# Optimization experiments

Measured on AMD Instinct MI355X. Metric: run time of the kernel, lower is better.

Reference implementation:

```python
import jax, jax.numpy as jnp
import numpy as np

H = 16
D_MODEL = 1024
D_K = D_MODEL // H  # 64, must equal embeddim


def setup_inputs() -> dict:
    key = jax.random.key(0)
    ks = jax.random.split(key, 20)
    B, S, D = 4, 1024, D_MODEL
    s = 0.02
    inp = {
        'query': jax.random.normal(ks[0], (B, S, D), jnp.float32),
        'key':   jax.random.normal(ks[1], (B, S, D), jnp.float32),
        'value': jax.random.normal(ks[2], (B, S, D), jnp.float32),
        'mask':  jnp.ones((B, S, S), jnp.int32),
        # four d_model x d_model projections (q, k, v, out)
        'wq': jax.random.normal(ks[3], (D, D), jnp.float32) * s, 'bq': jnp.zeros((D,), jnp.float32),
        'wk': jax.random.normal(ks[4], (D, D), jnp.float32) * s, 'bk': jnp.zeros((D,), jnp.float32),
        'wv': jax.random.normal(ks[5], (D, D), jnp.float32) * s, 'bv': jnp.zeros((D,), jnp.float32),
        'wo': jax.random.normal(ks[6], (D, D), jnp.float32) * s, 'bo': jnp.zeros((D,), jnp.float32),
        # per-head (embeddim=64) linears
        'spatial_w': jax.random.normal(ks[7], (D_K, D_K), jnp.float32) * s, 'spatial_b': jnp.zeros((D_K,), jnp.float32),
        'qproj_w':   jax.random.normal(ks[8], (D_K, D_K), jnp.float32) * s, 'qproj_b':   jnp.zeros((D_K,), jnp.float32),
        'kproj_w':   jax.random.normal(ks[9], (D_K, D_K), jnp.float32) * s, 'kproj_b':   jnp.zeros((D_K,), jnp.float32),
        'vlin_w':    jax.random.normal(ks[10], (D_K, D_K), jnp.float32) * s, 'vlin_b':    jnp.zeros((D_K,), jnp.float32),
        # channel_linear: Linear(1, 64)
        'chan_w': jax.random.normal(ks[11], (1, D_K), jnp.float32) * s, 'chan_b': jnp.zeros((D_K,), jnp.float32),
    }
    return inp


def reference(query, key, value, mask,
              wq, bq, wk, bk, wv, bv, wo, bo,
              spatial_w, spatial_b, qproj_w, qproj_b,
              kproj_w, kproj_b, vlin_w, vlin_b, chan_w, chan_b):
    B, S, D = query.shape
    # project and split heads -> [B, H, S, D_K]
    def heads(x, w, b):
        return (x @ w + b).reshape(B, S, H, D_K).transpose(0, 2, 1, 3)
    q = heads(query, wq, bq)
    k = heads(key, wk, bk)
    v = heads(value, wv, bv)

    q = jax.nn.elu(q @ spatial_w + spatial_b)
    q_refine = q @ qproj_w + qproj_b
    # channel gate: mean over channels -> Linear(1,64) -> matmul with raw key
    alpha = q_refine.mean(-1, keepdims=True) @ chan_w + chan_b        # [B,H,S,64]
    gate = jax.nn.sigmoid(jnp.einsum('bhqe,bhke->bhqk', alpha, k))    # [B,H,S,S]

    k2 = jax.nn.elu(k @ kproj_w + kproj_b)
    scores = jnp.einsum('bhqe,bhke->bhqk', q, k2) / jnp.sqrt(jnp.asarray(D_K, q.dtype))
    scores = scores * gate
    scores = jnp.where(mask[:, None] == 0, jnp.asarray(-1e9, scores.dtype), scores)
    p_attn = jax.nn.softmax(scores, axis=-1)

    v2 = jax.nn.elu(v @ vlin_w + vlin_b)
    x = jnp.einsum('bhqk,bhke->bhqe', p_attn, v2)                     # [B,H,S,64]
    x = x.transpose(0, 2, 1, 3).reshape(B, S, H * D_K)
    return x @ wo + bo
```

## Files before the change

### kernel.cpp

```cpp
#include <hip/hip_runtime.h>
#include <math.h>

#define D_MODEL 1024
#define NH 16
#define DK 64
#define S_LEN 1024
#define BATCH 4
#define MROWS (BATCH * S_LEN)

typedef short bf16x8 __attribute__((ext_vector_type(8)));
typedef float f32x4 __attribute__((ext_vector_type(4)));
typedef unsigned short u16;

__device__ __forceinline__ float elu1(float x) {
    return x > 0.f ? x : (expf(x) - 1.f);
}

__device__ __forceinline__ u16 f2bf(float f) {
    union { float f; unsigned u; } v; v.f = f;
    unsigned u = v.u;
    return (u16)((u + 0x7fffu + ((u >> 16) & 1u)) >> 16);
}

__device__ __forceinline__ float bf2f(u16 h) {
    union { unsigned u; float f; } v; v.u = ((unsigned)h) << 16;
    return v.f;
}

__device__ __forceinline__ unsigned pack2(float a, float b) {
    union { float f; unsigned u; } ua, ub; ua.f = a; ub.f = b;
    return ((ua.u + 0x8000u) >> 16) | ((ub.u + 0x8000u) & 0xffff0000u);
}

__device__ __forceinline__ void async16(const void* g, void* l) {
    __builtin_amdgcn_global_load_lds(
        (const __attribute__((address_space(1))) unsigned int*)g,
        (__attribute__((address_space(3))) unsigned int*)l,
        16, 0, 0);
}

__global__ __launch_bounds__(256) void cast_wt(
    const float* __restrict__ wq, const float* __restrict__ wk,
    const float* __restrict__ wv, const float* __restrict__ wo,
    u16* __restrict__ WT)
{
    __shared__ float T[64][65];
    const int z = blockIdx.z;
    const float* W = (z == 0) ? wq : ((z == 1) ? wk : ((z == 2) ? wv : wo));
    u16* O = WT + (size_t)z * D_MODEL * D_MODEL;
    const int tid = threadIdx.x;
    const int k0 = blockIdx.y * 64, n0 = blockIdx.x * 64;
    const int r = tid >> 4, c4 = (tid & 15) * 4;
    #pragma unroll
    for (int p = 0; p < 4; p++) {
        float4 v = *(const float4*)&W[(size_t)(k0 + r + p * 16) * D_MODEL + n0 + c4];
        T[r + p * 16][c4 + 0] = v.x; T[r + p * 16][c4 + 1] = v.y;
        T[r + p * 16][c4 + 2] = v.z; T[r + p * 16][c4 + 3] = v.w;
    }
    __syncthreads();
    #pragma unroll
    for (int p = 0; p < 4; p++) {
        const int i = r + p * 16;
        ushort4 o4;
        o4.x = f2bf(T[c4 + 0][i]); o4.y = f2bf(T[c4 + 1][i]);
        o4.z = f2bf(T[c4 + 2][i]); o4.w = f2bf(T[c4 + 3][i]);
        *(ushort4*)&O[(size_t)(n0 + i) * D_MODEL + k0 + c4] = o4;
    }
}

__global__ __launch_bounds__(256) void proj_gemm(
    const float* __restrict__ Xq, const float* __restrict__ Xk, const float* __restrict__ Xv,
    const u16* __restrict__ WTq, const u16* __restrict__ WTk, const u16* __restrict__ WTv,
    const float* __restrict__ bq, const float* __restrict__ bk, const float* __restrict__ bv,
    u16* __restrict__ Pbuf)
{
    __shared__ u16 As[128 * 32];
    __shared__ u16 Bs[128 * 32];

    const int z = blockIdx.z;
    const float* X = (z == 0) ? Xq : ((z == 1) ? Xk : Xv);
    const u16* WT = (z == 0) ? WTq : ((z == 1) ? WTk : WTv);
    const float* bias = (z == 0) ? bq : ((z == 1) ? bk : bv);
    u16* C = Pbuf + (size_t)z * MROWS * D_MODEL;

    const int tid = threadIdx.x;
    const int wave = tid >> 6, lane = tid & 63;
    const int col = lane & 15, quad = lane >> 4;
    const int wr = wave >> 1, wc = wave & 1;
    const int n0 = blockIdx.x * 128, r0 = blockIdx.y * 128;

    const int arow = tid >> 1, ahalf = tid & 1;
    const float* aptr = X + (size_t)(r0 + arow) * D_MODEL + ahalf * 16;
    u16* adst = As + arow * 32 + ahalf * 16;

    const int ch0 = 2 * wave, ch1 = 2 * wave + 1;
    const u16* bptr0 = WT + (size_t)(n0 + ch0 * 16 + (lane >> 2)) * D_MODEL + (lane & 3) * 8;
    const u16* bptr1 = WT + (size_t)(n0 + ch1 * 16 + (lane >> 2)) * D_MODEL + (lane & 3) * 8;
    u16* bdst0 = Bs + ch0 * 512;
    u16* bdst1 = Bs + ch1 * 512;

    f32x4 acc[4][4];
    #pragma unroll
    for (int i = 0; i < 4; i++)
        #pragma unroll
        for (int j = 0; j < 4; j++)
            acc[i][j] = (f32x4){0.f, 0.f, 0.f, 0.f};

    float4 f0 = *(const float4*)(aptr);
    float4 f1 = *(const float4*)(aptr + 4);
    float4 f2 = *(const float4*)(aptr + 8);
    float4 f3 = *(const float4*)(aptr + 12);

    for (int k0 = 0; k0 < D_MODEL; k0 += 32) {
        if (k0) __syncthreads();
        async16(bptr0 + k0, bdst0);
        async16(bptr1 + k0, bdst1);
        {
            uint4 p0, p1;
            p0.x = pack2(f0.x, f0.y); p0.y = pack2(f0.z, f0.w);
            p0.z = pack2(f1.x, f1.y); p0.w = pack2(f1.z, f1.w);
            p1.x = pack2(f2.x, f2.y); p1.y = pack2(f2.z, f2.w);
            p1.z = pack2(f3.x, f3.y); p1.w = pack2(f3.z, f3.w);
            *(uint4*)adst = p0;
            *(uint4*)(adst + 8) = p1;
        }
        if (k0 + 32 < D_MODEL) {
            const float* ap = aptr + k0 + 32;
            f0 = *(const float4*)(ap);
            f1 = *(const float4*)(ap + 4);
            f2 = *(const float4*)(ap + 8);
            f3 = *(const float4*)(ap + 12);
        }
        __syncthreads();
        const u16* Ab = As + (wr * 64 + col) * 32 + quad * 8;
        const u16* Bb = Bs + (wc * 64 + col) * 32 + quad * 8;
        bf16x8 af[4], bfr[4];
        #pragma unroll
        for (int mi = 0; mi < 4; mi++) af[mi] = *(const bf16x8*)(Ab + mi * 512);
        #pragma unroll
        for (int ni = 0; ni < 4; ni++) bfr[ni] = *(const bf16x8*)(Bb + ni * 512);
        #pragma unroll
        for (int mi = 0; mi < 4; mi++)
            #pragma unroll
            for (int ni = 0; ni < 4; ni++)
                acc[mi][ni] = __builtin_amdgcn_mfma_f32_16x16x32_bf16(af[mi], bfr[ni], acc[mi][ni], 0, 0, 0);
    }

    #pragma unroll
    for (int mi = 0; mi < 4; mi++)
        #pragma unroll
        for (int ni = 0; ni < 4; ni++) {
            const int gr = r0 + wr * 64 + mi * 16 + quad * 4;
            const int gc = n0 + wc * 64 + ni * 16 + col;
            const float bb = bias[gc];
            #pragma unroll
            for (int r = 0; r < 4; r++)
                C[(size_t)(gr + r) * D_MODEL + gc] = f2bf(acc[mi][ni][r] + bb);
        }
}

__global__ __launch_bounds__(256) void head_post(
    const u16* Pbuf, u16* QK2buf,
    const float* __restrict__ spatial_w, const float* __restrict__ spatial_b,
    const float* __restrict__ qproj_w, const float* __restrict__ qproj_b,
    const float* __restrict__ kproj_w, const float* __restrict__ kproj_b,
    const float* __restrict__ vlin_w, const float* __restrict__ vlin_b,
    const float* __restrict__ chan_w, const float* __restrict__ chan_b,
    u16* __restrict__ V2t, float* __restrict__ mB,
    float* __restrict__ uB, float* __restrict__ vB)
{
    __shared__ u16 Pl[64][72];
    __shared__ u16 W2t[64][72];
    __shared__ float auxA[64], auxB[64];
    __shared__ float auxS;

    const int z = blockIdx.z;
    const int h = blockIdx.x;
    const int r0 = blockIdx.y * 64;
    const u16* P = Pbuf + (size_t)z * MROWS * D_MODEL;
    const float* W2 = (z == 0) ? spatial_w : ((z == 1) ? kproj_w : vlin_w);
    const float* B2 = (z == 0) ? spatial_b : ((z == 1) ? kproj_b : vlin_b);

    const int tid = threadIdx.x;
    #pragma unroll
    for (int p = 0; p < 2; p++) {
        int idx = p * 256 + tid;
        int row = idx >> 3, seg = idx & 7;
        *(uint4*)&Pl[row][seg * 8] =
            *(const uint4*)&P[(size_t)(r0 + row) * D_MODEL + h * 64 + seg * 8];
    }
    #pragma unroll
    for (int p = 0; p < 4; p++) {
        int idx = p * 256 + tid;
        int f = idx >> 4, e4 = (idx & 15) * 4;
        float4 w4 = *(const float4*)&W2[f * 64 + e4];
        W2t[e4 + 0][f] = f2bf(w4.x); W2t[e4 + 1][f] = f2bf(w4.y);
        W2t[e4 + 2][f] = f2bf(w4.z); W2t[e4 + 3][f] = f2bf(w4.w);
    }
    if (z == 0) {
        if (tid < 64) {
            float s = 0.f;
            for (int e = 0; e < 64; e++) s += qproj_w[tid * 64 + e];
            auxA[tid] = s * (1.f / 64.f);
        }
        if (tid == 0) {
            float s = 0.f;
            for (int e = 0; e < 64; e++) s += qproj_b[e];
            auxS = s * (1.f / 64.f);
        }
    } else if (z == 1) {
        if (tid < 64) { auxA[tid] = chan_w[tid]; auxB[tid] = chan_b[tid]; }
    }
    __syncthreads();

    const int wave = tid >> 6, lane = tid & 63;
    const int col = lane & 15, quad = lane >> 4;
    bf16x8 a0 = *(const bf16x8*)&Pl[wave * 16 + col][quad * 8];
    bf16x8 a1 = *(const bf16x8*)&Pl[wave * 16 + col][32 + quad * 8];
    f32x4 acc[4];
    #pragma unroll
    for (int ni = 0; ni < 4; ni++) acc[ni] = (f32x4){0.f, 0.f, 0.f, 0.f};
    #pragma unroll
    for (int ni = 0; ni < 4; ni++) {
        bf16x8 b0 = *(const bf16x8*)&W2t[ni * 16 + col][quad * 8];
        bf16x8 b1 = *(const bf16x8*)&W2t[ni * 16 + col][32 + quad * 8];
        acc[ni] = __builtin_amdgcn_mfma_f32_16x16x32_bf16(a0, b0, acc[ni], 0, 0, 0);
        acc[ni] = __builtin_amdgcn_mfma_f32_16x16x32_bf16(a1, b1, acc[ni], 0, 0, 0);
    }
    float qs[4][4];
    #pragma unroll
    for (int ni = 0; ni < 4; ni++) {
        const float bb = B2[ni * 16 + col];
        #pragma unroll
        for (int r = 0; r < 4; r++) qs[ni][r] = elu1(acc[ni][r] + bb);
    }

    const int b = r0 >> 10;
    const int sloc = (r0 & 1023) + wave * 16 + quad * 4;
    const int grow = r0 + wave * 16 + quad * 4;

    if (z <= 1) {
        u16* Q = QK2buf + (size_t)z * MROWS * D_MODEL;
        #pragma unroll
        for (int ni = 0; ni < 4; ni++)
            #pragma unroll
            for (int r = 0; r < 4; r++)
                Q[(size_t)(grow + r) * D_MODEL + h * 64 + ni * 16 + col] = f2bf(qs[ni][r]);
    }
    if (z == 0) {
        #pragma unroll
        for (int r = 0; r < 4; r++) {
            float pm = 0.f;
            #pragma unroll
            for (int ni = 0; ni < 4; ni++) pm += qs[ni][r] * auxA[ni * 16 + col];
            pm += __shfl_xor(pm, 1);
            pm += __shfl_xor(pm, 2);
            pm += __shfl_xor(pm, 4);
            pm += __shfl_xor(pm, 8);
            if (col == 0)
                mB[((size_t)b * NH + h) * S_LEN + sloc + r] = pm + auxS;
        }
    } else if (z == 1) {
        const int row = tid >> 2, sub = tid & 3;
        float su = 0.f, sv = 0.f;
        for (int e = sub * 16; e < sub * 16 + 16; e++) {
            float p = bf2f(Pl[row][e]);
            su += p * auxA[e];
            sv += p * auxB[e];
        }
        su += __shfl_xor(su, 1); su += __shfl_xor(su, 2);
        sv += __shfl_xor(sv, 1); sv += __shfl_xor(sv, 2);
        if (sub == 0) {
            const size_t idx = ((size_t)b * NH + h) * S_LEN + (r0 & 1023) + row;
            uB[idx] = su;
            vB[idx] = sv;
        }
    } else {
        __syncthreads();
        #pragma unroll
        for (int ni = 0; ni < 4; ni++)
            #pragma unroll
            for (int r = 0; r < 4; r++)
                Pl[ni * 16 + col][wave * 16 + quad * 4 + r] = f2bf(qs[ni][r]);
        __syncthreads();
        #pragma unroll
        for (int p = 0; p < 2; p++) {
            int idx = p * 256 + tid;
            int d = idx >> 3, seg = idx & 7;
            *(uint4*)&V2t[(((size_t)b * NH + h) * DK + d) * S_LEN + (r0 & 1023) + seg * 8] =
                *(uint4*)&Pl[d][seg * 8];
        }
    }
}

__global__ __launch_bounds__(256) void attn_mfma(
    const u16* __restrict__ Qh, const u16* __restrict__ K2h, const u16* __restrict__ V2t,
    const float* __restrict__ Mq, const float* __restrict__ Uk, const float* __restrict__ Vk,
    const int* __restrict__ mask, u16* __restrict__ X)
{
    __shared__ u16 K2s[2][64][72];
    __shared__ u16 V2s[2][64][72];
    __shared__ u16 Ps[4][16][72];

    const int tid = threadIdx.x;
    const int wave = tid >> 6, lane = tid & 63;
    const int col = lane & 15, quad = lane >> 4;
    const int b = blockIdx.z, h = blockIdx.y;
    const int q0 = blockIdx.x * 64;
    const size_t hb = ((size_t)(b * NH + h)) * S_LEN * DK;
    const size_t sb = ((size_t)(b * NH + h)) * S_LEN;

    bf16x8 qf0, qf1;
    {
        const u16* qp = Qh + (size_t)(b * S_LEN + q0 + wave * 16 + col) * D_MODEL + h * 64 + quad * 8;
        qf0 = *(const bf16x8*)qp;
        qf1 = *(const bf16x8*)(qp + 32);
    }
    float mqv[4];
    #pragma unroll
    for (int r = 0; r < 4; r++)
        mqv[r] = Mq[sb + q0 + wave * 16 + quad * 4 + r];

    const int srow = tid >> 2, sseg = tid & 3;
    const u16* ksrc = K2h + (size_t)(b * S_LEN + srow) * D_MODEL + h * 64 + sseg * 16;
    const u16* vsrc = V2t + hb + (size_t)srow * S_LEN + sseg * 16;
    const int* mrow = mask + (size_t)b * S_LEN * S_LEN
                    + (size_t)(q0 + wave * 16 + quad * 4) * S_LEN + col;

    uint4 ka = *(const uint4*)(ksrc);
    uint4 kb = *(const uint4*)(ksrc + 8);
    uint4 va = *(const uint4*)(vsrc);
    uint4 vb = *(const uint4*)(vsrc + 8);
    float ku[4], kv[4];
    int mk[4][4];
    #pragma unroll
    for (int nb = 0; nb < 4; nb++) {
        ku[nb] = Uk[sb + nb * 16 + col];
        kv[nb] = Vk[sb + nb * 16 + col];
        #pragma unroll
        for (int r = 0; r < 4; r++) mk[nb][r] = mrow[(size_t)r * S_LEN + nb * 16];
    }

    float psum[4] = {0.f, 0.f, 0.f, 0.f};
    f32x4 o[4];
    #pragma unroll
    for (int nb = 0; nb < 4; nb++) o[nb] = (f32x4){0.f, 0.f, 0.f, 0.f};

    for (int t = 0; t < 16; t++) {
        const int bsel = t & 1;
        *(uint4*)&K2s[bsel][srow][sseg * 16]     = ka;
        *(uint4*)&K2s[bsel][srow][sseg * 16 + 8] = kb;
        *(uint4*)&V2s[bsel][srow][sseg * 16]     = va;
        *(uint4*)&V2s[bsel][srow][sseg * 16 + 8] = vb;
        __syncthreads();

        float kun[4], kvn[4];
        int mkn[4][4];
        if (t < 15) {
            const int k1 = (t + 1) * 64;
            const u16* ks = ksrc + (size_t)k1 * D_MODEL;
            const u16* vs = vsrc + k1;
            ka = *(const uint4*)(ks);
            kb = *(const uint4*)(ks + 8);
            va = *(const uint4*)(vs);
            vb = *(const uint4*)(vs + 8);
            #pragma unroll
            for (int nb = 0; nb < 4; nb++) {
                kun[nb] = Uk[sb + k1 + nb * 16 + col];
                kvn[nb] = Vk[sb + k1 + nb * 16 + col];
                #pragma unroll
                for (int r = 0; r < 4; r++)
                    mkn[nb][r] = mrow[k1 + (size_t)r * S_LEN + nb * 16];
            }
        }

        f32x4 sc[4];
        #pragma unroll
        for (int nb = 0; nb < 4; nb++) {
            bf16x8 b0 = *(const bf16x8*)&K2s[bsel][nb * 16 + col][quad * 8];
            bf16x8 b1 = *(const bf16x8*)&K2s[bsel][nb * 16 + col][32 + quad * 8];
            f32x4 c = (f32x4){0.f, 0.f, 0.f, 0.f};
            c = __builtin_amdgcn_mfma_f32_16x16x32_bf16(qf0, b0, c, 0, 0, 0);
            c = __builtin_amdgcn_mfma_f32_16x16x32_bf16(qf1, b1, c, 0, 0, 0);
            sc[nb] = c;
        }

        #pragma unroll
        for (int nb = 0; nb < 4; nb++) {
            #pragma unroll
            for (int r = 0; r < 4; r++) {
                float g = 1.f / (1.f + __expf(-(mqv[r] * ku[nb] + kv[nb])));
                float sv = sc[nb][r] * 0.125f * g;
                sv = mk[nb][r] ? sv : -30.f;
                float p = __expf(sv);
                psum[r] += p;
                Ps[wave][quad * 4 + r][nb * 16 + col] = f2bf(p);
            }
        }
        __builtin_amdgcn_s_waitcnt(0xc07f);
        bf16x8 a0 = *(const bf16x8*)&Ps[wave][col][quad * 8];
        bf16x8 a1 = *(const bf16x8*)&Ps[wave][col][32 + quad * 8];

        #pragma unroll
        for (int nb = 0; nb < 4; nb++) {
            bf16x8 b0 = *(const bf16x8*)&V2s[bsel][nb * 16 + col][quad * 8];
            bf16x8 b1 = *(const bf16x8*)&V2s[bsel][nb * 16 + col][32 + quad * 8];
            o[nb] = __builtin_amdgcn_mfma_f32_16x16x32_bf16(a0, b0, o[nb], 0, 0, 0);
            o[nb] = __builtin_amdgcn_mfma_f32_16x16x32_bf16(a1, b1, o[nb], 0, 0, 0);
        }

        if (t < 15) {
            #pragma unroll
            for (int nb = 0; nb < 4; nb++) {
                ku[nb] = kun[nb]; kv[nb] = kvn[nb];
                #pragma unroll
                for (int r = 0; r < 4; r++) mk[nb][r] = mkn[nb][r];
            }
        }
    }

    #pragma unroll
    for (int r = 0; r < 4; r++) {
        float t = psum[r];
        t += __shfl_xor(t, 1);
        t += __shfl_xor(t, 2);
        t += __shfl_xor(t, 4);
        t += __shfl_xor(t, 8);
        float inv = 1.f / t;
        u16* xp = X + (size_t)(b * S_LEN + q0 + wave * 16 + quad * 4 + r) * D_MODEL + h * 64 + col;
        #pragma unroll
        for (int nb = 0; nb < 4; nb++)
            xp[nb * 16] = f2bf(o[nb][r] * inv);
    }
}

__global__ __launch_bounds__(256) void out_gemm(
    const u16* __restrict__ A, const u16* __restrict__ WT,
    const float* __restrict__ bias, float* __restrict__ C)
{
    __shared__ u16 As[128 * 32];
    __shared__ u16 Bs[128 * 32];

    const int tid = threadIdx.x;
    const int wave = tid >> 6, lane = tid & 63;
    const int col = lane & 15, quad = lane >> 4;
    const int wr = wave >> 1, wc = wave & 1;
    const int n0 = blockIdx.x * 128, r0 = blockIdx.y * 128;

    const int ch0 = 2 * wave, ch1 = 2 * wave + 1;
    const u16* aptr0 = A + (size_t)(r0 + ch0 * 16 + (lane >> 2)) * D_MODEL + (lane & 3) * 8;
    const u16* aptr1 = A + (size_t)(r0 + ch1 * 16 + (lane >> 2)) * D_MODEL + (lane & 3) * 8;
    const u16* bptr0 = WT + (size_t)(n0 + ch0 * 16 + (lane >> 2)) * D_MODEL + (lane & 3) * 8;
    const u16* bptr1 = WT + (size_t)(n0 + ch1 * 16 + (lane >> 2)) * D_MODEL + (lane & 3) * 8;
    u16* adst0 = As + ch0 * 512;
    u16* adst1 = As + ch1 * 512;
    u16* bdst0 = Bs + ch0 * 512;
    u16* bdst1 = Bs + ch1 * 512;

    f32x4 acc[4][4];
    #pragma unroll
    for (int i = 0; i < 4; i++)
        #pragma unroll
        for (int j = 0; j < 4; j++)
            acc[i][j] = (f32x4){0.f, 0.f, 0.f, 0.f};

    for (int k0 = 0; k0 < D_MODEL; k0 += 32) {
        if (k0) __syncthreads();
        async16(aptr0 + k0, adst0);
        async16(aptr1 + k0, adst1);
        async16(bptr0 + k0, bdst0);
        async16(bptr1 + k0, bdst1);
        __syncthreads();
        const u16* Ab = As + (wr * 64 + col) * 32 + quad * 8;
        const u16* Bb = Bs + (wc * 64 + col) * 32 + quad * 8;
        bf16x8 af[4], bfr[4];
        #pragma unroll
        for (int mi = 0; mi < 4; mi++) af[mi] = *(const bf16x8*)(Ab + mi * 512);
        #pragma unroll
        for (int ni = 0; ni < 4; ni++) bfr[ni] = *(const bf16x8*)(Bb + ni * 512);
        #pragma unroll
        for (int mi = 0; mi < 4; mi++)
            #pragma unroll
            for (int ni = 0; ni < 4; ni++)
                acc[mi][ni] = __builtin_amdgcn_mfma_f32_16x16x32_bf16(af[mi], bfr[ni], acc[mi][ni], 0, 0, 0);
    }

    #pragma unroll
    for (int mi = 0; mi < 4; mi++)
        #pragma unroll
        for (int ni = 0; ni < 4; ni++) {
            const int gr = r0 + wr * 64 + mi * 16 + quad * 4;
            const int gc = n0 + wc * 64 + ni * 16 + col;
            const float bb = bias[gc];
            #pragma unroll
            for (int r = 0; r < 4; r++)
                C[(size_t)(gr + r) * D_MODEL + gc] = acc[mi][ni][r] + bb;
        }
}

extern "C" void kernel_launch(void* const* d_in, const int* in_sizes, int n_in,
                              void* d_out, int out_size, void* d_ws, size_t ws_size,
                              hipStream_t stream) {
    (void)in_sizes; (void)n_in; (void)out_size; (void)ws_size;
    const float* query = (const float*)d_in[0];
    const float* key_  = (const float*)d_in[1];
    const float* value = (const float*)d_in[2];
    const int*   mask  = (const int*)d_in[3];
    const float* wq = (const float*)d_in[4];  const float* bq = (const float*)d_in[5];
    const float* wk = (const float*)d_in[6];  const float* bk = (const float*)d_in[7];
    const float* wv = (const float*)d_in[8];  const float* bv = (const float*)d_in[9];
    const float* wo = (const float*)d_in[10]; const float* bo = (const float*)d_in[11];
    const float* spatial_w = (const float*)d_in[12]; const float* spatial_b = (const float*)d_in[13];
    const float* qproj_w   = (const float*)d_in[14]; const float* qproj_b   = (const float*)d_in[15];
    const float* kproj_w   = (const float*)d_in[16]; const float* kproj_b   = (const float*)d_in[17];
    const float* vlin_w    = (const float*)d_in[18]; const float* vlin_b    = (const float*)d_in[19];
    const float* chan_w    = (const float*)d_in[20]; const float* chan_b    = (const float*)d_in[21];
    float* out = (float*)d_out;

    char* ws = (char*)d_ws;
    u16* Pbuf = (u16*)ws;
    u16* WT   = (u16*)(ws + ((size_t)24 << 20));
    u16* V2t  = (u16*)(ws + ((size_t)32 << 20));
    float* mB = (float*)(ws + ((size_t)40 << 20));
    float* uB = mB + (size_t)BATCH * NH * S_LEN;
    float* vB = uB + (size_t)BATCH * NH * S_LEN;
    u16* Qh = Pbuf;
    u16* K2 = Pbuf + (size_t)MROWS * D_MODEL;
    u16* Xb = Pbuf + (size_t)2 * MROWS * D_MODEL;
    const size_t WSZ = (size_t)D_MODEL * D_MODEL;

    cast_wt<<<dim3(16, 16, 4), 256, 0, stream>>>(wq, wk, wv, wo, WT);
    proj_gemm<<<dim3(8, 32, 3), 256, 0, stream>>>(query, key_, value,
        WT, WT + WSZ, WT + 2 * WSZ, bq, bk, bv, Pbuf);
    head_post<<<dim3(NH, MROWS / 64, 3), 256, 0, stream>>>(Pbuf, Pbuf,
        spatial_w, spatial_b, qproj_w, qproj_b, kproj_w, kproj_b,
        vlin_w, vlin_b, chan_w, chan_b, V2t, mB, uB, vB);
    attn_mfma<<<dim3(S_LEN / 64, NH, BATCH), 256, 0, stream>>>(Qh, K2, V2t, mB, uB, vB, mask, Xb);
    out_gemm<<<dim3(8, 32), 256, 0, stream>>>(Xb, WT + 3 * WSZ, bo, out);
}
```

Baseline: 319.4 us.

## Fuse per-head post-projection into the QKV projection GEMM epilogue

Merges head_post into the projection GEMM. Each wave's 64x64 output tile is one head slice, so the 64x64 per-head linear, ELU, channel-gate reductions and V transpose now run in the epilogue straight from registers and shared memory. This removes one kernel launch and the bf16 round-trip of the three projection outputs through global memory. It also folds the 1/sqrt(dk) scale into Qh and shrinks attention LDS by single-buffering V2s and reusing the spare K2s buffer for P, at the cost of an extra barrier per tile and more register pressure in the fused GEMM.

Result: slower. 330.4 us (+3.4%).

```diff
diff --git a/kernel.cpp b/kernel.cpp
--- a/kernel.cpp
+++ b/kernel.cpp
@@ -20,11 +20,6 @@
     union { float f; unsigned u; } v; v.f = f;
     unsigned u = v.u;
     return (u16)((u + 0x7fffu + ((u >> 16) & 1u)) >> 16);
-}
-
-__device__ __forceinline__ float bf2f(u16 h) {
-    union { unsigned u; float f; } v; v.u = ((unsigned)h) << 16;
-    return v.f;
 }
 
 __device__ __forceinline__ unsigned pack2(float a, float b) {
@@ -68,26 +63,66 @@
     }
 }
 
-__global__ __launch_bounds__(256) void proj_gemm(
+__global__ __launch_bounds__(256) void proj_fused(
     const float* __restrict__ Xq, const float* __restrict__ Xk, const float* __restrict__ Xv,
     const u16* __restrict__ WTq, const u16* __restrict__ WTk, const u16* __restrict__ WTv,
     const float* __restrict__ bq, const float* __restrict__ bk, const float* __restrict__ bv,
-    u16* __restrict__ Pbuf)
+    const float* __restrict__ spatial_w, const float* __restrict__ spatial_b,
+    const float* __restrict__ qproj_w, const float* __restrict__ qproj_b,
+    const float* __restrict__ kproj_w, const float* __restrict__ kproj_b,
+    const float* __restrict__ vlin_w, const float* __restrict__ vlin_b,
+    const float* __restrict__ chan_w, const float* __restrict__ chan_b,
+    u16* __restrict__ Qh, u16* __restrict__ K2, u16* __restrict__ V2t,
+    float* __restrict__ mB, float* __restrict__ uB, float* __restrict__ vB)
 {
-    __shared__ u16 As[128 * 32];
-    __shared__ u16 Bs[128 * 32];
+    __shared__ __align__(16) u16 smem[23040];
+    __shared__ float auxA[64];
+    __shared__ float auxS;
+
+    u16* As = smem;
+    u16* Bs = smem + 4096;
+    u16* W2t = smem + 18432;
 
     const int z = blockIdx.z;
     const float* X = (z == 0) ? Xq : ((z == 1) ? Xk : Xv);
     const u16* WT = (z == 0) ? WTq : ((z == 1) ? WTk : WTv);
-    const float* bias = (z == 0) ? bq : ((z == 1) ? bk : bv);
-    u16* C = Pbuf + (size_t)z * MROWS * D_MODEL;
+    const float* B1 = (z == 0) ? bq : ((z == 1) ? bk : bv);
+    const float* W2 = (z == 0) ? spatial_w : ((z == 1) ? kproj_w : vlin_w);
+    const float* B2 = (z == 0) ? spatial_b : ((z == 1) ? kproj_b : vlin_b);
 
     const int tid = threadIdx.x;
     const int wave = tid >> 6, lane = tid & 63;
     const int col = lane & 15, quad = lane >> 4;
     const int wr = wave >> 1, wc = wave & 1;
     const int n0 = blockIdx.x * 128, r0 = blockIdx.y * 128;
+    const int hh = blockIdx.x * 2 + wc;
+
+    #pragma unroll
+    for (int p = 0; p < 4; p++) {
+        int idx = p * 256 + tid;
+        int f = idx >> 4, e4 = (idx & 15) * 4;
+        float4 w4 = *(const float4*)&W2[f * 64 + e4];
+        W2t[(e4 + 0) * 72 + f] = f2bf(w4.x);
+        W2t[(e4 + 1) * 72 + f] = f2bf(w4.y);
+        W2t[(e4 + 2) * 72 + f] = f2bf(w4.z);
+        W2t[(e4 + 3) * 72 + f] = f2bf(w4.w);
+    }
+    if (z == 0) {
+        {
+            int row = tid >> 2, part = tid & 3;
+            float s = 0.f;
+            for (int e = part * 16; e < part * 16 + 16; e++) s += qproj_w[row * 64 + e];
+            s += __shfl_xor(s, 1);
+            s += __shfl_xor(s, 2);
+            if (part == 0) auxA[row] = s * (1.f / 64.f);
+        }
+        if (tid < 64) {
+            float s = qproj_b[tid];
+            #pragma unroll
+            for (int m = 1; m < 64; m <<= 1) s += __shfl_xor(s, m);
+            if (tid == 0) auxS = s * (1.f / 64.f);
+        }
+    }
 
     const int arow = tid >> 1, ahalf = tid & 1;
     const float* aptr = X + (size_t)(r0 + arow) * D_MODEL + ahalf * 16;
@@ -146,150 +181,139 @@
                 acc[mi][ni] = __builtin_amdgcn_mfma_f32_16x16x32_bf16(af[mi], bfr[ni], acc[mi][ni], 0, 0, 0);
     }
 
+    float b1v[4];
+    #pragma unroll
+    for (int ni = 0; ni < 4; ni++) b1v[ni] = B1[hh * 64 + ni * 16 + col];
+
+    const int rbase = r0 + wr * 64;
+    const int b = rbase >> 10;
+    const int s0 = rbase & 1023;
+    const size_t svecbase = ((size_t)b * NH + hh) * S_LEN;
+
+    if (z == 1) {
+        float cw[4], cb[4];
+        #pragma unroll
+        for (int ni = 0; ni < 4; ni++) { cw[ni] = chan_w[ni * 16 + col]; cb[ni] = chan_b[ni * 16 + col]; }
+        #pragma unroll
+        for (int mi = 0; mi < 4; mi++)
+            #pragma unroll
+            for (int r = 0; r < 4; r++) {
+                float su = 0.f, sv = 0.f;
+                #pragma unroll
+                for (int ni = 0; ni < 4; ni++) {
+                    float p = acc[mi][ni][r] + b1v[ni];
+                    su += p * cw[ni];
+                    sv += p * cb[ni];
+                }
+                su += __shfl_xor(su, 1); su += __shfl_xor(su, 2);
+                su += __shfl_xor(su, 4); su += __shfl_xor(su, 8);
+                sv += __shfl_xor(sv, 1); sv += __shfl_xor(sv, 2);
+                sv += __shfl_xor(sv, 4); sv += __shfl_xor(sv, 8);
+                if (col == 0) {
+                    const size_t idx = svecbase + s0 + mi * 16 + quad * 4 + r;
+                    uB[idx] = su;
+                    vB[idx] = sv;
+                }
+            }
+    }
+
+    __syncthreads();
+
+    u16* Pw = smem + wave * 4608;
     #pragma unroll
     for (int mi = 0; mi < 4; mi++)
         #pragma unroll
+        for (int ni = 0; ni < 4; ni++)
+            #pragma unroll
+            for (int r = 0; r < 4; r++)
+                Pw[(mi * 16 + quad * 4 + r) * 72 + ni * 16 + col] =
+                    f2bf(acc[mi][ni][r] + b1v[ni]);
+
+    __builtin_amdgcn_s_waitcnt(0xc07f);
+
+    bf16x8 af2[4][2], bf2r[4][2];
+    #pragma unroll
+    for (int mi = 0; mi < 4; mi++) {
+        af2[mi][0] = *(const bf16x8*)&Pw[(mi * 16 + col) * 72 + quad * 8];
+        af2[mi][1] = *(const bf16x8*)&Pw[(mi * 16 + col) * 72 + 32 + quad * 8];
+    }
+    #pragma unroll
+    for (int ni = 0; ni < 4; ni++) {
+        bf2r[ni][0] = *(const bf16x8*)&W2t[(ni * 16 + col) * 72 + quad * 8];
+        bf2r[ni][1] = *(const bf16x8*)&W2t[(ni * 16 + col) * 72 + 32 + quad * 8];
+    }
+    f32x4 out2[4][4];
+    #pragma unroll
+    for (int mi = 0; mi < 4; mi++)
+        #pragma unroll
         for (int ni = 0; ni < 4; ni++) {
-            const int gr = r0 + wr * 64 + mi * 16 + quad * 4;
-            const int gc = n0 + wc * 64 + ni * 16 + col;
-            const float bb = bias[gc];
+            f32x4 c = (f32x4){0.f, 0.f, 0.f, 0.f};
+            c = __builtin_amdgcn_mfma_f32_16x16x32_bf16(af2[mi][0], bf2r[ni][0], c, 0, 0, 0);
+            c = __builtin_amdgcn_mfma_f32_16x16x32_bf16(af2[mi][1], bf2r[ni][1], c, 0, 0, 0);
+            out2[mi][ni] = c;
+        }
+
+    float b2v[4];
+    #pragma unroll
+    for (int ni = 0; ni < 4; ni++) b2v[ni] = B2[ni * 16 + col];
+    float qs[4][4][4];
+    #pragma unroll
+    for (int mi = 0; mi < 4; mi++)
+        #pragma unroll
+        for (int ni = 0; ni < 4; ni++)
             #pragma unroll
             for (int r = 0; r < 4; r++)
-                C[(size_t)(gr + r) * D_MODEL + gc] = f2bf(acc[mi][ni][r] + bb);
-        }
-}
-
-__global__ __launch_bounds__(256) void head_post(
-    const u16* Pbuf, u16* QK2buf,
-    const float* __restrict__ spatial_w, const float* __restrict__ spatial_b,
-    const float* __restrict__ qproj_w, const float* __restrict__ qproj_b,
-    const float* __restrict__ kproj_w, const float* __restrict__ kproj_b,
-    const float* __restrict__ vlin_w, const float* __restrict__ vlin_b,
-    const float* __restrict__ chan_w, const float* __restrict__ chan_b,
-    u16* __restrict__ V2t, float* __restrict__ mB,
-    float* __restrict__ uB, float* __restrict__ vB)
-{
-    __shared__ u16 Pl[64][72];
-    __shared__ u16 W2t[64][72];
-    __shared__ float auxA[64], auxB[64];
-    __shared__ float auxS;
-
-    const int z = blockIdx.z;
-    const int h = blockIdx.x;
-    const int r0 = blockIdx.y * 64;
-    const u16* P = Pbuf + (size_t)z * MROWS * D_MODEL;
-    const float* W2 = (z == 0) ? spatial_w : ((z == 1) ? kproj_w : vlin_w);
-    const float* B2 = (z == 0) ? spatial_b : ((z == 1) ? kproj_b : vlin_b);
-
-    const int tid = threadIdx.x;
-    #pragma unroll
-    for (int p = 0; p < 2; p++) {
-        int idx = p * 256 + tid;
-        int row = idx >> 3, seg = idx & 7;
-        *(uint4*)&Pl[row][seg * 8] =
-            *(const uint4*)&P[(size_t)(r0 + row) * D_MODEL + h * 64 + seg * 8];
-    }
-    #pragma unroll
-    for (int p = 0; p < 4; p++) {
-        int idx = p * 256 + tid;
-        int f = idx >> 4, e4 = (idx & 15) * 4;
-        float4 w4 = *(const float4*)&W2[f * 64 + e4];
-        W2t[e4 + 0][f] = f2bf(w4.x); W2t[e4 + 1][f] = f2bf(w4.y);
-        W2t[e4 + 2][f] = f2bf(w4.z); W2t[e4 + 3][f] = f2bf(w4.w);
-    }
+                qs[mi][ni][r] = elu1(out2[mi][ni][r] + b2v[ni]);
+
     if (z == 0) {
-        if (tid < 64) {
-            float s = 0.f;
-            for (int e = 0; e < 64; e++) s += qproj_w[tid * 64 + e];
-            auxA[tid] = s * (1.f / 64.f);
-        }
-        if (tid == 0) {
-            float s = 0.f;
-            for (int e = 0; e < 64; e++) s += qproj_b[e];
-            auxS = s * (1.f / 64.f);
-        }
+        float aw[4];
+        #pragma unroll
+        for (int ni = 0; ni < 4; ni++) aw[ni] = auxA[ni * 16 + col];
+        #pragma unroll
+        for (int mi = 0; mi < 4; mi++)
+            #pragma unroll
+            for (int r = 0; r < 4; r++) {
+                float pm = 0.f;
+                #pragma unroll
+                for (int ni = 0; ni < 4; ni++) pm += qs[mi][ni][r] * aw[ni];
+                pm += __shfl_xor(pm, 1); pm += __shfl_xor(pm, 2);
+                pm += __shfl_xor(pm, 4); pm += __shfl_xor(pm, 8);
+                if (col == 0)
+                    mB[svecbase + s0 + mi * 16 + quad * 4 + r] = pm + auxS;
+            }
+        #pragma unroll
+        for (int mi = 0; mi < 4; mi++)
+            #pragma unroll
+            for (int ni = 0; ni < 4; ni++)
+                #pragma unroll
+                for (int r = 0; r < 4; r++)
+                    Qh[(size_t)(rbase + mi * 16 + quad * 4 + r) * D_MODEL
+                       + hh * 64 + ni * 16 + col] = f2bf(qs[mi][ni][r] * 0.125f);
     } else if (z == 1) {
-        if (tid < 64) { auxA[tid] = chan_w[tid]; auxB[tid] = chan_b[tid]; }
-    }
-    __syncthreads();
-
-    const int wave = tid >> 6, lane = tid & 63;
-    const int col = lane & 15, quad = lane >> 4;
-    bf16x8 a0 = *(const bf16x8*)&Pl[wave * 16 + col][quad * 8];
-    bf16x8 a1 = *(const bf16x8*)&Pl[wave * 16 + col][32 + quad * 8];
-    f32x4 acc[4];
-    #pragma unroll
-    for (int ni = 0; ni < 4; ni++) acc[ni] = (f32x4){0.f, 0.f, 0.f, 0.f};
-    #pragma unroll
-    for (int ni = 0; ni < 4; ni++) {
-        bf16x8 b0 = *(const bf16x8*)&W2t[ni * 16 + col][quad * 8];
-        bf16x8 b1 = *(const bf16x8*)&W2t[ni * 16 + col][32 + quad * 8];
-        acc[ni] = __builtin_amdgcn_mfma_f32_16x16x32_bf16(a0, b0, acc[ni], 0, 0, 0);
-        acc[ni] = __builtin_amdgcn_mfma_f32_16x16x32_bf16(a1, b1, acc[ni], 0, 0, 0);
-    }
-    float qs[4][4];
-    #pragma unroll
-    for (int ni = 0; ni < 4; ni++) {
-        const float bb = B2[ni * 16 + col];
-        #pragma unroll
-        for (int r = 0; r < 4; r++) qs[ni][r] = elu1(acc[ni][r] + bb);
-    }
-
-    const int b = r0 >> 10;
-    const int sloc = (r0 & 1023) + wave * 16 + quad * 4;
-    const int grow = r0 + wave * 16 + quad * 4;
-
-    if (z <= 1) {
-        u16* Q = QK2buf + (size_t)z * MROWS * D_MODEL;
-        #pragma unroll
-        for (int ni = 0; ni < 4; ni++)
-            #pragma unroll
-            for (int r = 0; r < 4; r++)
-                Q[(size_t)(grow + r) * D_MODEL + h * 64 + ni * 16 + col] = f2bf(qs[ni][r]);
-    }
-    if (z == 0) {
-        #pragma unroll
-        for (int r = 0; r < 4; r++) {
-            float pm = 0.f;
-            #pragma unroll
-            for (int ni = 0; ni < 4; ni++) pm += qs[ni][r] * auxA[ni * 16 + col];
-            pm += __shfl_xor(pm, 1);
-            pm += __shfl_xor(pm, 2);
-            pm += __shfl_xor(pm, 4);
-            pm += __shfl_xor(pm, 8);
-            if (col == 0)
-                mB[((size_t)b * NH + h) * S_LEN + sloc + r] = pm + auxS;
-        }
-    } else if (z == 1) {
-        const int row = tid >> 2, sub = tid & 3;
-        float su = 0.f, sv = 0.f;
-        for (int e = sub * 16; e < sub * 16 + 16; e++) {
-            float p = bf2f(Pl[row][e]);
-            su += p * auxA[e];
-            sv += p * auxB[e];
-        }
-        su += __shfl_xor(su, 1); su += __shfl_xor(su, 2);
-        sv += __shfl_xor(sv, 1); sv += __shfl_xor(sv, 2);
-        if (sub == 0) {
-            const size_t idx = ((size_t)b * NH + h) * S_LEN + (r0 & 1023) + row;
-            uB[idx] = su;
-            vB[idx] = sv;
-        }
+        #pragma unroll
+        for (int mi = 0; mi < 4; mi++)
+            #pragma unroll
+            for (int ni = 0; ni < 4; ni++)
+                #pragma unroll
+                for (int r = 0; r < 4; r++)
+                    K2[(size_t)(rbase + mi * 16 + quad * 4 + r) * D_MODEL
+                       + hh * 64 + ni * 16 + col] = f2bf(qs[mi][ni][r]);
     } else {
-        __syncthreads();
-        #pragma unroll
-        for (int ni = 0; ni < 4; ni++)
-            #pragma unroll
-            for (int r = 0; r < 4; r++)
-                Pl[ni * 16 + col][wave * 16 + quad * 4 + r] = f2bf(qs[ni][r]);
-        __syncthreads();
-        #pragma unroll
-        for (int p = 0; p < 2; p++) {
-            int idx = p * 256 + tid;
-            int d = idx >> 3, seg = idx & 7;
-            *(uint4*)&V2t[(((size_t)b * NH + h) * DK + d) * S_LEN + (r0 & 1023) + seg * 8] =
-                *(uint4*)&Pl[d][seg * 8];
-        }
+        __builtin_amdgcn_s_waitcnt(0xc07f);
+        #pragma unroll
+        for (int mi = 0; mi < 4; mi++)
+            #pragma unroll
+            for (int ni = 0; ni < 4; ni++)
+                #pragma unroll
+                for (int r = 0; r < 4; r++)
+                    Pw[(ni * 16 + col) * 72 + mi * 16 + quad * 4 + r] = f2bf(qs[mi][ni][r]);
+        __builtin_amdgcn_s_waitcnt(0xc07f);
+        const int d = lane;
+        u16* dst = V2t + (((size_t)b * NH + hh) * DK + d) * S_LEN + s0;
+        const u16* srcp = Pw + d * 72;
+        #pragma unroll
+        for (int seg = 0; seg < 8; seg++)
+            *(uint4*)(dst + seg * 8) = *(const uint4*)(srcp + seg * 8);
     }
 }
 
@@ -299,8 +323,7 @@
     const int* __restrict__ mask, u16* __restrict__ X)
 {
     __shared__ u16 K2s[2][64][72];
-    __shared__ u16 V2s[2][64][72];
-    __shared__ u16 Ps[4][16][72];
+    __shared__ u16 V2s[64][72];
 
     const int tid = threadIdx.x;
     const int wave = tid >> 6, lane = tid & 63;
@@ -350,8 +373,8 @@
         const int bsel = t & 1;
         *(uint4*)&K2s[bsel][srow][sseg * 16]     = ka;
         *(uint4*)&K2s[bsel][srow][sseg * 16 + 8] = kb;
-        *(uint4*)&V2s[bsel][srow][sseg * 16]     = va;
-        *(uint4*)&V2s[bsel][srow][sseg * 16 + 8] = vb;
+        *(uint4*)&V2s[srow][sseg * 16]           = va;
+        *(uint4*)&V2s[srow][sseg * 16 + 8]       = vb;
         __syncthreads();
 
         float kun[4], kvn[4];
@@ -385,29 +408,31 @@
             sc[nb] = c;
         }
 
+        u16* Ps = &K2s[1 - bsel][wave * 16][0];
         #pragma unroll
         for (int nb = 0; nb < 4; nb++) {
             #pragma unroll
             for (int r = 0; r < 4; r++) {
                 float g = 1.f / (1.f + __expf(-(mqv[r] * ku[nb] + kv[nb])));
-                float sv = sc[nb][r] * 0.125f * g;
+                float sv = sc[nb][r] * g;
                 sv = mk[nb][r] ? sv : -30.f;
                 float p = __expf(sv);
                 psum[r] += p;
-                Ps[wave][quad * 4 + r][nb * 16 + col] = f2bf(p);
+                Ps[(quad * 4 + r) * 72 + nb * 16 + col] = f2bf(p);
             }
         }
         __builtin_amdgcn_s_waitcnt(0xc07f);
-        bf16x8 a0 = *(const bf16x8*)&Ps[wave][col][quad * 8];
-        bf16x8 a1 = *(const bf16x8*)&Ps[wave][col][32 + quad * 8];
+        bf16x8 a0 = *(const bf16x8*)&Ps[col * 72 + quad * 8];
+        bf16x8 a1 = *(const bf16x8*)&Ps[col * 72 + 32 + quad * 8];
 
         #pragma unroll
         for (int nb = 0; nb < 4; nb++) {
-            bf16x8 b0 = *(const bf16x8*)&V2s[bsel][nb * 16 + col][quad * 8];
-            bf16x8 b1 = *(const bf16x8*)&V2s[bsel][nb * 16 + col][32 + quad * 8];
+            bf16x8 b0 = *(const bf16x8*)&V2s[nb * 16 + col][quad * 8];
+            bf16x8 b1 = *(const bf16x8*)&V2s[nb * 16 + col][32 + quad * 8];
             o[nb] = __builtin_amdgcn_mfma_f32_16x16x32_bf16(a0, b0, o[nb], 0, 0, 0);
             o[nb] = __builtin_amdgcn_mfma_f32_16x16x32_bf16(a1, b1, o[nb], 0, 0, 0);
         }
+        __syncthreads();
 
         if (t < 15) {
             #pragma unroll
@@ -518,23 +543,22 @@
     float* out = (float*)d_out;
 
     char* ws = (char*)d_ws;
-    u16* Pbuf = (u16*)ws;
-    u16* WT   = (u16*)(ws + ((size_t)24 << 20));
-    u16* V2t  = (u16*)(ws + ((size_t)32 << 20));
+    u16* Qh  = (u16*)ws;
+    u16* K2  = (u16*)(ws + ((size_t)8  << 20));
+    u16* Xb  = (u16*)(ws + ((size_t)16 << 20));
+    u16* WT  = (u16*)(ws + ((size_t)24 << 20));
+    u16* V2t = (u16*)(ws + ((size_t)32 << 20));
     float* mB = (float*)(ws + ((size_t)40 << 20));
     float* uB = mB + (size_t)BATCH * NH * S_LEN;
     float* vB = uB + (size_t)BATCH * NH * S_LEN;
-    u16* Qh = Pbuf;
-    u16* K2 = Pbuf + (size_t)MROWS * D_MODEL;
-    u16* Xb = Pbuf + (size_t)2 * MROWS * D_MODEL;
     const size_t WSZ = (size_t)D_MODEL * D_MODEL;
 
     cast_wt<<<dim3(16, 16, 4), 256, 0, stream>>>(wq, wk, wv, wo, WT);
-    proj_gemm<<<dim3(8, 32, 3), 256, 0, stream>>>(query, key_, value,
-        WT, WT + WSZ, WT + 2 * WSZ, bq, bk, bv, Pbuf);
-    head_post<<<dim3(NH, MROWS / 64, 3), 256, 0, stream>>>(Pbuf, Pbuf,
+    proj_fused<<<dim3(8, 32, 3), 256, 0, stream>>>(query, key_, value,
+        WT, WT + WSZ, WT + 2 * WSZ, bq, bk, bv,
         spatial_w, spatial_b, qproj_w, qproj_b, kproj_w, kproj_b,
-        vlin_w, vlin_b, chan_w, chan_b, V2t, mB, uB, vB);
+        vlin_w, vlin_b, chan_w, chan_b,
+        Qh, K2, V2t, mB, uB, vB);
     attn_mfma<<<dim3(S_LEN / 64, NH, BATCH), 256, 0, stream>>>(Qh, K2, V2t, mB, uB, vB, mask, Xb);
     out_gemm<<<dim3(8, 32), 256, 0, stream>>>(Xb, WT + 3 * WSZ, bo, out);
 }
```
